# Optimization experiments

Hardware: AMD Instinct MI355X
Metric: run time of the kernel (lower is better)

The kernel has to match this reference:

```python
import jax, jax.numpy as jnp
import numpy as np

BATCH, T, S, M = 512, 4096, 64, 125  # batch, seq_len, n_states, emission alphabet (5^3)


def setup_inputs() -> dict:
    key = jax.random.key(0)
    k1, k2, k3, k4 = jax.random.split(key, 4)
    obs = jax.random.randint(k1, (BATCH, T), 0, M)
    x = jax.nn.one_hot(obs, M, dtype=jnp.float32)            # [B, T, M] one-hot emissions
    I = jax.nn.softmax(jax.random.normal(k2, (1, S)))        # initial state distribution [1, S]
    A = jax.nn.softmax(jax.random.normal(k3, (S, S)), axis=-1)   # transition matrix, rows sum to 1
    Bm = jax.nn.softmax(jax.random.normal(k4, (M, S)), axis=0)   # emission matrix, cols sum to 1
    return {"x": x, "I": I, "A": A, "Bm": Bm}


def reference(x, I, A, Bm):
    """HMM forward algorithm with per-step normalization (default scaling branch of CgpHmmCell).

    Returns the accumulated log-likelihood [B, 1].
    """
    xT = jnp.swapaxes(x, 0, 1)  # [T, B, M] for scan over time

    # t = 1: R = I (broadcast over batch), old_loglik = 0
    E0 = xT[0] @ Bm                                  # [B, S]
    u0 = E0 * I                                      # unscaled alpha
    Z0 = jnp.sum(u0, axis=1, keepdims=True)          # [B, 1]
    carry0 = (u0 / Z0, jnp.log(Z0))

    def step(carry, x_t):
        alpha, ll = carry
        R = alpha @ A                                # [B, S] transition
        E = x_t @ Bm                                 # [B, S] emission lookup (one-hot matmul)
        u = E * R
        Z = jnp.sum(u, axis=1, keepdims=True)        # per-sequence scaling factor
        return (u / Z, ll + jnp.log(Z)), None

    (alpha, loglik), _ = jax.lax.scan(step, carry0, xT[1:])
    return loglik
```

## Files before the change

kernel.cpp:

```cpp
#include <hip/hip_runtime.h>


#define BATCH 512
#define T 4096
#define S 64
#define M 125
#define CHUNKP 4
#define BURNP 2
#define NPACK 6
#define WPB 4
#define NQ 2
#define RB 56.0f
#define SCALEF 7.205759403792794e16f

typedef __attribute__((ext_vector_type(8))) short bf16x8;
typedef __attribute__((ext_vector_type(4))) float f32x4;

union BFU { unsigned u[4]; bf16x8 v; };

__device__ __forceinline__ unsigned pk_trunc(float a, float b) {
    return (__float_as_uint(b) & 0xFFFF0000u) | (__float_as_uint(a) >> 16);
}
__device__ __forceinline__ unsigned pk_rne(float a, float b) {
    unsigned ua = __float_as_uint(a); ua += 0x7FFFu + ((ua >> 16) & 1u);
    unsigned ub = __float_as_uint(b); ub += 0x7FFFu + ((ub >> 16) & 1u);
    return (ub & 0xFFFF0000u) | (ua >> 16);
}

__global__ __launch_bounds__(256) void extract_obs(const float4* __restrict__ x4,
                                                   unsigned char* __restrict__ obs) {
    const long long i0 = ((long long)blockIdx.x * 256 + threadIdx.x) * 4;
    float4 v[4];
#pragma unroll
    for (int t = 0; t < 4; ++t) v[t] = x4[i0 + t];
#pragma unroll
    for (int t = 0; t < 4; ++t) {
        float4 vv = v[t];
        if (vv.x != 0.f || vv.y != 0.f || vv.z != 0.f || vv.w != 0.f) {
            long long e = (i0 + t) * 4;
            if (vv.x != 0.f) { long long r = (e + 0) / M; obs[r] = (unsigned char)(e + 0 - r * M); }
            if (vv.y != 0.f) { long long r = (e + 1) / M; obs[r] = (unsigned char)(e + 1 - r * M); }
            if (vv.z != 0.f) { long long r = (e + 2) / M; obs[r] = (unsigned char)(e + 2 - r * M); }
            if (vv.w != 0.f) { long long r = (e + 3) / M; obs[r] = (unsigned char)(e + 3 - r * M); }
        }
    }
}

__global__ __launch_bounds__(256) void hmm_mfma(const unsigned char* __restrict__ obs,
                                                const float* __restrict__ Iv,
                                                const float* __restrict__ A,
                                                const float* __restrict__ Bm,
                                                float* __restrict__ out) {
    __shared__ __align__(16) float BmL[M * S];
    __shared__ __align__(16) float ILds[S];

    const int tid = threadIdx.x, lane = tid & 63;
    const int s = lane & 15, g = lane >> 4;

    for (int i = tid; i < M * S; i += WPB * 64) BmL[i] = Bm[i];
    if (tid < S) ILds[tid] = Iv[tid];
    __syncthreads();

    BFU Af[4][2];
#pragma unroll
    for (int mt = 0; mt < 4; ++mt)
#pragma unroll
        for (int kf = 0; kf < 2; ++kf)
#pragma unroll
            for (int j2 = 0; j2 < 4; ++j2) {
                int p0 = 32 * kf + 16 * (j2 >> 1) + 4 * g + 2 * (j2 & 1);
                Af[mt][kf].u[j2] = pk_rne(A[(size_t)p0 * S + mt * 16 + s],
                                          A[(size_t)(p0 + 1) * S + mt * 16 + s]);
            }

    const int W = blockIdx.x * WPB + (tid >> 6);
    const int seq = W >> 2, quarter = W & 3;
    const unsigned long long* orow = (const unsigned long long*)(obs + (size_t)seq * T);

    int idx0[NQ];
    unsigned long long u[NQ], un[NQ];
    BFU Bf[NQ][2];
    float S0v[NQ], swv[NQ];
#pragma unroll
    for (int q = 0; q < NQ; ++q) {
        int chunk = quarter * 32 + q * 16 + s;
        idx0[q] = chunk * CHUNKP - BURNP;
        u[q] = orow[idx0[q] < 0 ? 0 : idx0[q]];
        S0v[q] = 0.f; swv[q] = 1.f;
#pragma unroll
        for (int kf = 0; kf < 2; ++kf)
#pragma unroll
            for (int j = 0; j < 4; ++j) Bf[q][kf].u[j] = 0x3F803F80u;
    }

    for (int p = 0; p < NPACK; ++p) {
#pragma unroll
        for (int q = 0; q < NQ; ++q) {
            int in_ = idx0[q] + p + 1;
            in_ = in_ < 0 ? 0 : (in_ > T / 8 - 1 ? T / 8 - 1 : in_);
            un[q] = orow[in_];
        }
        const bool ovp = (quarter == 0) && (p == BURNP);
        const bool massp = (p == BURNP - 1) || (p == NPACK - 1);
#pragma unroll
        for (int k = 0; k < 8; ++k) {
#pragma unroll
            for (int q = 0; q < NQ; ++q) {
                const int o = (int)((u[q] >> (8 * k)) & 255ull);
                const float* br = &BmL[o << 6];
                f32x4 E[4];
#pragma unroll
                for (int mt = 0; mt < 4; ++mt)
                    E[mt] = *(const f32x4*)&br[mt * 16 + g * 4];
                float w[4][4];
#pragma unroll
                for (int mt = 0; mt < 4; ++mt) {
                    f32x4 zr = {0.f, 0.f, 0.f, 0.f};
                    f32x4 z0 = __builtin_amdgcn_mfma_f32_16x16x32_bf16(Af[mt][0].v, Bf[q][0].v, zr, 0, 0, 0);
                    f32x4 z1 = __builtin_amdgcn_mfma_f32_16x16x32_bf16(Af[mt][1].v, Bf[q][1].v, zr, 0, 0, 0);
#pragma unroll
                    for (int r = 0; r < 4; ++r) w[mt][r] = (z0[r] + z1[r]) * E[mt][r];
                }
                if (ovp && k == 0 && q == 0) {
                    const bool c0 = (s == 0);
#pragma unroll
                    for (int mt = 0; mt < 4; ++mt)
#pragma unroll
                        for (int r = 0; r < 4; ++r)
                            w[mt][r] = c0 ? ILds[mt * 16 + g * 4 + r] * E[mt][r] : w[mt][r];
                }
                if (k == 7 && massp) {
                    float swl = 0.f;
#pragma unroll
                    for (int mt = 0; mt < 4; ++mt)
#pragma unroll
                        for (int r = 0; r < 4; ++r) swl += w[mt][r];
                    swl += __shfl_xor(swl, 16);
                    swl += __shfl_xor(swl, 32);
                    swv[q] = swl;
                }
#pragma unroll
                for (int kf = 0; kf < 2; ++kf)
#pragma unroll
                    for (int j2 = 0; j2 < 4; ++j2) {
                        int mt = 2 * kf + (j2 >> 1), pr = j2 & 1;
                        float v0 = w[mt][2 * pr], v1 = w[mt][2 * pr + 1];
                        if (k == 7) { v0 *= SCALEF; v1 *= SCALEF; }
                        Bf[q][kf].u[j2] = pk_trunc(v0, v1);
                    }
            }
        }
        if (p == BURNP - 1) {
#pragma unroll
            for (int q = 0; q < NQ; ++q) {
                const bool ch0 = (quarter == 0) && (q == 0) && (s == 0);
                S0v[q] = ch0 ? (3.0f * RB) : (__log2f(swv[q]) + 4.0f * RB);
            }
        }
#pragma unroll
        for (int q = 0; q < NQ; ++q) u[q] = un[q];
    }

    float tot = 0.f;
#pragma unroll
    for (int q = 0; q < NQ; ++q)
        tot += __log2f(swv[q]) - S0v[q];
    tot += __shfl_xor(tot, 1);
    tot += __shfl_xor(tot, 2);
    tot += __shfl_xor(tot, 4);
    tot += __shfl_xor(tot, 8);
    if (lane == 0)
        atomicAdd(out + seq, tot * 0.6931471805599453f);
}

extern "C" void kernel_launch(void* const* d_in, const int* in_sizes, int n_in,
                              void* d_out, int out_size, void* d_ws, size_t ws_size,
                              hipStream_t stream) {
    const float* x  = (const float*)d_in[0];
    const float* I  = (const float*)d_in[1];
    const float* A  = (const float*)d_in[2];
    const float* Bm = (const float*)d_in[3];
    float* out = (float*)d_out;
    unsigned char* obs = (unsigned char*)d_ws;

    hipMemsetAsync(out, 0, (size_t)out_size * sizeof(float), stream);
    extract_obs<<<64000, 256, 0, stream>>>((const float4*)x, obs);
    hmm_mfma<<<512, WPB * 64, 0, stream>>>(obs, I, A, Bm, out);
}
```

Before: 1.314 ms.

## Fuse one-hot observation extraction into the HMM MFMA kernel via wave ballots

Drops the separate extract_obs kernel and the workspace byte array. The HMM kernel now reads the one-hot x rows itself, recovers each observation index with wave-wide ballots and count-trailing-zeros, stages the packed indices in LDS, and interleaves this extraction with the MFMA recurrence. Each wave now handles one 16-chunk group with 8 packs of 8 steps each (64 steps per chunk) instead of two groups with 4-pack chunks. That removes a kernel launch and the intermediate write/read, and overlaps streaming the 1 GB input with compute. The cost is heavier per-wave work, more register pressure from the load buffers, and less independent MFMA work per wave now that the two-chain interleave is gone.

Measured after the change: 1.309 ms. Within noise of the previous version (-0.4%).

```diff
diff --git a/kernel.cpp b/kernel.cpp
--- a/kernel.cpp
+++ b/kernel.cpp
@@ -5,11 +5,9 @@
 #define T 4096
 #define S 64
 #define M 125
-#define CHUNKP 4
+#define NPACK 10
 #define BURNP 2
-#define NPACK 6
 #define WPB 4
-#define NQ 2
 #define RB 56.0f
 #define SCALEF 7.205759403792794e16f
 
@@ -27,34 +25,16 @@
     return (ub & 0xFFFF0000u) | (ua >> 16);
 }
 
-__global__ __launch_bounds__(256) void extract_obs(const float4* __restrict__ x4,
-                                                   unsigned char* __restrict__ obs) {
-    const long long i0 = ((long long)blockIdx.x * 256 + threadIdx.x) * 4;
-    float4 v[4];
-#pragma unroll
-    for (int t = 0; t < 4; ++t) v[t] = x4[i0 + t];
-#pragma unroll
-    for (int t = 0; t < 4; ++t) {
-        float4 vv = v[t];
-        if (vv.x != 0.f || vv.y != 0.f || vv.z != 0.f || vv.w != 0.f) {
-            long long e = (i0 + t) * 4;
-            if (vv.x != 0.f) { long long r = (e + 0) / M; obs[r] = (unsigned char)(e + 0 - r * M); }
-            if (vv.y != 0.f) { long long r = (e + 1) / M; obs[r] = (unsigned char)(e + 1 - r * M); }
-            if (vv.z != 0.f) { long long r = (e + 2) / M; obs[r] = (unsigned char)(e + 2 - r * M); }
-            if (vv.w != 0.f) { long long r = (e + 3) / M; obs[r] = (unsigned char)(e + 3 - r * M); }
-        }
-    }
-}
-
-__global__ __launch_bounds__(256) void hmm_mfma(const unsigned char* __restrict__ obs,
-                                                const float* __restrict__ Iv,
-                                                const float* __restrict__ A,
-                                                const float* __restrict__ Bm,
-                                                float* __restrict__ out) {
+__global__ __launch_bounds__(256) void hmm_fused(const float* __restrict__ x,
+                                                 const float* __restrict__ Iv,
+                                                 const float* __restrict__ A,
+                                                 const float* __restrict__ Bm,
+                                                 float* __restrict__ out) {
     __shared__ __align__(16) float BmL[M * S];
     __shared__ __align__(16) float ILds[S];
-
-    const int tid = threadIdx.x, lane = tid & 63;
+    __shared__ unsigned long long ulds[WPB * 16 * NPACK];
+
+    const int tid = threadIdx.x, wv = tid >> 6, lane = tid & 63;
     const int s = lane & 15, g = lane >> 4;
 
     for (int i = tid; i < M * S; i += WPB * 64) BmL[i] = Bm[i];
@@ -73,98 +53,139 @@
                                           A[(size_t)(p0 + 1) * S + mt * 16 + s]);
             }
 
-    const int W = blockIdx.x * WPB + (tid >> 6);
-    const int seq = W >> 2, quarter = W & 3;
-    const unsigned long long* orow = (const unsigned long long*)(obs + (size_t)seq * T);
-
-    int idx0[NQ];
-    unsigned long long u[NQ], un[NQ];
-    BFU Bf[NQ][2];
-    float S0v[NQ], swv[NQ];
-#pragma unroll
-    for (int q = 0; q < NQ; ++q) {
-        int chunk = quarter * 32 + q * 16 + s;
-        idx0[q] = chunk * CHUNKP - BURNP;
-        u[q] = orow[idx0[q] < 0 ? 0 : idx0[q]];
-        S0v[q] = 0.f; swv[q] = 1.f;
-#pragma unroll
-        for (int kf = 0; kf < 2; ++kf)
-#pragma unroll
-            for (int j = 0; j < 4; ++j) Bf[q][kf].u[j] = 0x3F803F80u;
+    const int W = blockIdx.x * WPB + wv;
+    const int seq = W >> 2, wq = W & 3;
+    const float* xs = x + (size_t)seq * T * M;
+    unsigned long long* myu = &ulds[wv * 16 * NPACK];
+    const int base = wq * 1024;
+
+    float bufA[16], bufB[16];
+
+    auto issue16 = [&](int r0a, int r0b) {
+#pragma unroll
+        for (int j = 0; j < 8; ++j) {
+            unsigned ra = (unsigned)((r0a + j) * 125);
+            unsigned rb = (unsigned)((r0b + j) * 125);
+            bufA[j] = xs[ra + lane];       bufB[j] = xs[ra + 61 + lane];
+            bufA[8 + j] = xs[rb + lane];   bufB[8 + j] = xs[rb + 61 + lane];
+        }
+    };
+    auto ext8 = [&](int jb) -> unsigned long long {
+        unsigned long long acc = 0;
+#pragma unroll
+        for (int j = 0; j < 8; ++j) {
+            unsigned long long mA = __ballot(bufA[jb + j] != 0.0f);
+            unsigned long long mB = __ballot(bufB[jb + j] != 0.0f);
+            int o = mA ? (int)__builtin_ctzll(mA) : 61 + (int)__builtin_ctzll(mB);
+            acc |= (unsigned long long)o << (8 * j);
+        }
+        return acc;
+    };
+    auto put = [&](int st, int pt, unsigned long long v) {
+        if (lane == st) myu[st * NPACK + pt] = v;
+    };
+
+    {
+        int pa = base - 16, pb = base - 8;
+        if (pa < 0) pa = 0;
+        if (pb < 0) pb = 0;
+        issue16(pa, pb);
+        for (int gi = 0; gi <= 16; ++gi) {
+            unsigned long long a0 = ext8(0), a1 = ext8(8);
+            if (gi < 16) {
+                int ni = gi + 1;
+                if (ni <= 8) { int i = ni - 1; issue16(base + (2 * i) * 64 + 48, base + (2 * i + 1) * 64 + 48); }
+                else         { int i = ni - 9; issue16(base + (2 * i) * 64 + 56, base + (2 * i + 1) * 64 + 56); }
+            } else {
+                issue16(base + 0, base + 64);
+            }
+            if (gi == 0) {
+                put(0, 0, a0); put(0, 1, a1);
+            } else if (gi <= 8) {
+                int i = gi - 1;
+                put(2 * i, 8, a0);     put(2 * i + 1, 0, a0);
+                put(2 * i + 1, 8, a1); if (2 * i + 2 <= 15) put(2 * i + 2, 0, a1);
+            } else {
+                int i = gi - 9;
+                put(2 * i, 9, a0);     put(2 * i + 1, 1, a0);
+                put(2 * i + 1, 9, a1); if (2 * i + 2 <= 15) put(2 * i + 2, 1, a1);
+            }
+        }
     }
 
+    BFU Bf[2];
+#pragma unroll
+    for (int kf = 0; kf < 2; ++kf)
+#pragma unroll
+        for (int j = 0; j < 4; ++j) Bf[kf].u[j] = 0x3F803F80u;
+
+    float S0v = 0.f, swv = 1.f;
+
     for (int p = 0; p < NPACK; ++p) {
-#pragma unroll
-        for (int q = 0; q < NQ; ++q) {
-            int in_ = idx0[q] + p + 1;
-            in_ = in_ < 0 ? 0 : (in_ > T / 8 - 1 ? T / 8 - 1 : in_);
-            un[q] = orow[in_];
-        }
-        const bool ovp = (quarter == 0) && (p == BURNP);
-        const bool massp = (p == BURNP - 1) || (p == NPACK - 1);
-#pragma unroll
+        unsigned long long uv = myu[s * NPACK + p];
+        const bool exsl = (p < 6);
         for (int k = 0; k < 8; ++k) {
-#pragma unroll
-            for (int q = 0; q < NQ; ++q) {
-                const int o = (int)((u[q] >> (8 * k)) & 255ull);
-                const float* br = &BmL[o << 6];
-                f32x4 E[4];
+            if (exsl) {
+                unsigned long long a0 = ext8(0), a1 = ext8(8);
+                int np = (k == 7) ? p + 1 : p, nk = (k + 1) & 7;
+                if (np < 6)
+                    issue16(base + (2 * nk) * 64 + 8 * np,
+                            base + (2 * nk + 1) * 64 + 8 * np);
+                put(2 * k, p + 2, a0);
+                put(2 * k + 1, p + 2, a1);
+            }
+            const int o = (int)(uv & 255ull);
+            uv >>= 8;
+            const float* br = &BmL[o << 6];
+            f32x4 E[4];
+#pragma unroll
+            for (int mt = 0; mt < 4; ++mt)
+                E[mt] = *(const f32x4*)&br[mt * 16 + g * 4];
+            float w[4][4];
+#pragma unroll
+            for (int mt = 0; mt < 4; ++mt) {
+                f32x4 zr = {0.f, 0.f, 0.f, 0.f};
+                f32x4 z0 = __builtin_amdgcn_mfma_f32_16x16x32_bf16(Af[mt][0].v, Bf[0].v, zr, 0, 0, 0);
+                f32x4 z1 = __builtin_amdgcn_mfma_f32_16x16x32_bf16(Af[mt][1].v, Bf[1].v, zr, 0, 0, 0);
+#pragma unroll
+                for (int r = 0; r < 4; ++r) w[mt][r] = (z0[r] + z1[r]) * E[mt][r];
+            }
+            if (p == BURNP && k == 0 && wq == 0) {
+                const bool c0 = (s == 0);
 #pragma unroll
                 for (int mt = 0; mt < 4; ++mt)
-                    E[mt] = *(const f32x4*)&br[mt * 16 + g * 4];
-                float w[4][4];
-#pragma unroll
-                for (int mt = 0; mt < 4; ++mt) {
-                    f32x4 zr = {0.f, 0.f, 0.f, 0.f};
-                    f32x4 z0 = __builtin_amdgcn_mfma_f32_16x16x32_bf16(Af[mt][0].v, Bf[q][0].v, zr, 0, 0, 0);
-                    f32x4 z1 = __builtin_amdgcn_mfma_f32_16x16x32_bf16(Af[mt][1].v, Bf[q][1].v, zr, 0, 0, 0);
-#pragma unroll
-                    for (int r = 0; r < 4; ++r) w[mt][r] = (z0[r] + z1[r]) * E[mt][r];
+#pragma unroll
+                    for (int r = 0; r < 4; ++r)
+                        w[mt][r] = c0 ? ILds[mt * 16 + g * 4 + r] * E[mt][r] : w[mt][r];
+            }
+            if (k == 7 && (p == BURNP - 1 || p == NPACK - 1)) {
+                float swl = 0.f;
+#pragma unroll
+                for (int mt = 0; mt < 4; ++mt)
+#pragma unroll
+                    for (int r = 0; r < 4; ++r) swl += w[mt][r];
+                swl += __shfl_xor(swl, 16);
+                swl += __shfl_xor(swl, 32);
+                swv = swl;
+            }
+#pragma unroll
+            for (int kf = 0; kf < 2; ++kf)
+#pragma unroll
+                for (int j2 = 0; j2 < 4; ++j2) {
+                    int mt = 2 * kf + (j2 >> 1), pr = j2 & 1;
+                    float v0 = w[mt][2 * pr], v1 = w[mt][2 * pr + 1];
+                    if (k == 7) { v0 *= SCALEF; v1 *= SCALEF; }
+                    Bf[kf].u[j2] = pk_trunc(v0, v1);
                 }
-                if (ovp && k == 0 && q == 0) {
-                    const bool c0 = (s == 0);
-#pragma unroll
-                    for (int mt = 0; mt < 4; ++mt)
-#pragma unroll
-                        for (int r = 0; r < 4; ++r)
-                            w[mt][r] = c0 ? ILds[mt * 16 + g * 4 + r] * E[mt][r] : w[mt][r];
-                }
-                if (k == 7 && massp) {
-                    float swl = 0.f;
-#pragma unroll
-                    for (int mt = 0; mt < 4; ++mt)
-#pragma unroll
-                        for (int r = 0; r < 4; ++r) swl += w[mt][r];
-                    swl += __shfl_xor(swl, 16);
-                    swl += __shfl_xor(swl, 32);
-                    swv[q] = swl;
-                }
-#pragma unroll
-                for (int kf = 0; kf < 2; ++kf)
-#pragma unroll
-                    for (int j2 = 0; j2 < 4; ++j2) {
-                        int mt = 2 * kf + (j2 >> 1), pr = j2 & 1;
-                        float v0 = w[mt][2 * pr], v1 = w[mt][2 * pr + 1];
-                        if (k == 7) { v0 *= SCALEF; v1 *= SCALEF; }
-                        Bf[q][kf].u[j2] = pk_trunc(v0, v1);
-                    }
-            }
         }
         if (p == BURNP - 1) {
-#pragma unroll
-            for (int q = 0; q < NQ; ++q) {
-                const bool ch0 = (quarter == 0) && (q == 0) && (s == 0);
-                S0v[q] = ch0 ? (3.0f * RB) : (__log2f(swv[q]) + 4.0f * RB);
-            }
-        }
-#pragma unroll
-        for (int q = 0; q < NQ; ++q) u[q] = un[q];
+            const bool ch0 = (wq == 0) && (s == 0);
+            S0v = ch0 ? ((float)(NPACK - 1 - BURNP) * RB)
+                      : (__log2f(swv) + (float)(NPACK - BURNP) * RB);
+        }
     }
 
-    float tot = 0.f;
-#pragma unroll
-    for (int q = 0; q < NQ; ++q)
-        tot += __log2f(swv[q]) - S0v[q];
+    float tot = __log2f(swv) - S0v;
     tot += __shfl_xor(tot, 1);
     tot += __shfl_xor(tot, 2);
     tot += __shfl_xor(tot, 4);
@@ -181,9 +202,8 @@
     const float* A  = (const float*)d_in[2];
     const float* Bm = (const float*)d_in[3];
     float* out = (float*)d_out;
-    unsigned char* obs = (unsigned char*)d_ws;
+    (void)d_ws; (void)ws_size;
 
     hipMemsetAsync(out, 0, (size_t)out_size * sizeof(float), stream);
-    extract_obs<<<64000, 256, 0, stream>>>((const float4*)x, obs);
-    hmm_mfma<<<512, WPB * 64, 0, stream>>>(obs, I, A, Bm, out);
-}
+    hmm_fused<<<(BATCH * 4) / WPB, WPB * 64, 0, stream>>>(x, I, A, Bm, out);
+}
```
